# Kernel tuning notes

Measured on AMD Instinct MI355X. Metric: run time of the kernel, lower is better.

The kernel has to match this reference:

```python
import jax, jax.numpy as jnp
import numpy as np

# ---- Cl(4,1) Cayley table (conformal GA: metric +,+,+,+,-) ----
_METRIC = (1.0, 1.0, 1.0, 1.0, -1.0)

def _reorder_sign(a, b):
    # sign from counting swaps to bring blade product to canonical order
    a >>= 1
    s = 0
    while a:
        s += bin(a & b).count("1")
        a >>= 1
    return -1.0 if (s & 1) else 1.0

def _build_cayley():
    C = np.zeros((32, 32, 32), dtype=np.float32)
    for a in range(32):
        for b in range(32):
            s = _reorder_sign(a, b)
            common = a & b
            for i in range(5):
                if (common >> i) & 1:
                    s *= _METRIC[i]
            C[a, b, a ^ b] += s
    return C

CAYLEY = _build_cayley()  # [32,32,32]; out_k = sum_ij C[i,j,k] x_i y_j

EPS = 1e-8

def normalize_cl41(x):
    n = jnp.sqrt(jnp.sum(x * x, axis=-1, keepdims=True))
    return x / (n + EPS)


def setup_inputs() -> dict:
    key = jax.random.key(0)
    k_x, k_wi, k_bi, k_wo, k_bo = jax.random.split(key, 5)
    B, S, D, H = 64, 2048, 6, 8
    x = jax.random.normal(k_x, (B, S, D), dtype=jnp.float32)
    W_in = jax.random.normal(k_wi, (D, H * 32), dtype=jnp.float32) * (1.0 / np.sqrt(D))
    b_in = jax.random.normal(k_bi, (H * 32,), dtype=jnp.float32) * 0.01
    W_out = jax.random.normal(k_wo, (H * 32, 32), dtype=jnp.float32) * (1.0 / np.sqrt(H * 32))
    b_out = jax.random.normal(k_bo, (32,), dtype=jnp.float32) * 0.01
    return {"x": x, "W_in": W_in, "b_in": b_in, "W_out": W_out, "b_out": b_out}


def reference(x, W_in, b_in, W_out, b_out):
    B, S, D = x.shape
    H = W_in.shape[1] // 32
    C = jnp.asarray(CAYLEY)
    # project inputs to per-channel multivectors: (B,S,H,32)
    u = (x @ W_in + b_in).reshape(B, S, H, 32)
    # initial rotor state: identity (scalar blade = 1)
    psi0 = jnp.zeros((B, H, 32), dtype=x.dtype).at[..., 0].set(1.0)

    def step(psi, u_t):  # u_t: (B,H,32)
        delta = normalize_cl41(u_t.at[..., 0].add(1.0))
        psi = normalize_cl41(jnp.einsum("bhi,bhj,ijk->bhk", delta, psi, C))
        return psi, psi

    _, psi_seq = jax.lax.scan(step, psi0, jnp.swapaxes(u, 0, 1))  # (S,B,H,32)
    out = normalize_cl41(psi_seq.reshape(S, B, H * 32) @ W_out + b_out)  # (S,B,32)
    return jnp.swapaxes(out, 0, 1)  # (B,S,32)
```

## Files before the change

kernel.cpp:

```cpp
#include <hip/hip_runtime.h>
#include <hip/hip_bf16.h>
#include <stdint.h>

#define BB 64
#define SS 2048
#define DD 6
#define HH 8
#define NCH 512
#define CHUNKS 256
#define LCH 8

typedef unsigned short ushort_t;
typedef __attribute__((ext_vector_type(8))) __bf16 bf16x8;
typedef __attribute__((ext_vector_type(4))) float f32x4;

struct SignTab { float s[32][32]; };

constexpr int popc5_c(unsigned v) {
    int c = 0;
    for (int i = 0; i < 5; ++i) c += (v >> i) & 1u;
    return c;
}

constexpr SignTab make_signs() {
    SignTab t{};
    for (int a = 0; a < 32; ++a) {
        for (int b = 0; b < 32; ++b) {
            int cnt = 0;
            unsigned aa = ((unsigned)a) >> 1;
            while (aa) { cnt += popc5_c(aa & (unsigned)b); aa >>= 1; }
            if ((a & b) & 16) cnt += 1;
            t.s[a][b] = (cnt & 1) ? -1.0f : 1.0f;
        }
    }
    return t;
}

constexpr SignTab SGN = make_signs();

__device__ __forceinline__ void gp_cl41(const float* __restrict__ a,
                                        const float* __restrict__ b,
                                        float* __restrict__ o) {
#pragma unroll
    for (int k = 0; k < 32; ++k) o[k] = 0.0f;
#pragma unroll
    for (int i = 0; i < 32; ++i) {
#pragma unroll
        for (int k = 0; k < 32; ++k) {
            o[k] = fmaf(SGN.s[i][i ^ k] * a[i], b[i ^ k], o[k]);
        }
    }
}

__device__ __forceinline__ float sumsq32(const float* v) {
    float n0 = 0.f, n1 = 0.f, n2 = 0.f, n3 = 0.f;
#pragma unroll
    for (int k = 0; k < 32; k += 4) {
        n0 = fmaf(v[k+0], v[k+0], n0);
        n1 = fmaf(v[k+1], v[k+1], n1);
        n2 = fmaf(v[k+2], v[k+2], n2);
        n3 = fmaf(v[k+3], v[k+3], n3);
    }
    return (n0 + n1) + (n2 + n3);
}

__device__ __forceinline__ float rsq(float n) {
    return __builtin_amdgcn_rsqf(n);
}

__device__ __forceinline__ uint32_t f2bf_rne(float f) {
    uint32_t u = __float_as_uint(f);
    return (u + 0x7FFFu + ((u >> 16) & 1u)) >> 16;
}

__device__ __forceinline__ void loadp(const float4* __restrict__ a, int stride,
                                      int idx, float* __restrict__ v) {
#pragma unroll
    for (int m = 0; m < 8; ++m) {
        float4 t = a[m * stride + idx];
        v[4*m] = t.x; v[4*m+1] = t.y; v[4*m+2] = t.z; v[4*m+3] = t.w;
    }
}
__device__ __forceinline__ void storep(float4* __restrict__ a, int stride,
                                       int idx, const float* __restrict__ v) {
#pragma unroll
    for (int m = 0; m < 8; ++m)
        a[m * stride + idx] = make_float4(v[4*m], v[4*m+1], v[4*m+2], v[4*m+3]);
}

__device__ __forceinline__ void make_delta2(const float4* __restrict__ sW,
                                            const float* __restrict__ xv,
                                            float* __restrict__ dl0,
                                            float* __restrict__ dl1) {
#pragma unroll
    for (int j4 = 0; j4 < 8; ++j4) {
        float4 bv = sW[48 + j4];
        dl0[4*j4+0] = bv.x; dl0[4*j4+1] = bv.y; dl0[4*j4+2] = bv.z; dl0[4*j4+3] = bv.w;
        dl1[4*j4+0] = bv.x; dl1[4*j4+1] = bv.y; dl1[4*j4+2] = bv.z; dl1[4*j4+3] = bv.w;
    }
#pragma unroll
    for (int d = 0; d < 6; ++d) {
        float a0 = xv[d], a1 = xv[6 + d];
#pragma unroll
        for (int j4 = 0; j4 < 8; ++j4) {
            float4 w = sW[d * 8 + j4];
            dl0[4*j4+0] = fmaf(a0, w.x, dl0[4*j4+0]);
            dl0[4*j4+1] = fmaf(a0, w.y, dl0[4*j4+1]);
            dl0[4*j4+2] = fmaf(a0, w.z, dl0[4*j4+2]);
            dl0[4*j4+3] = fmaf(a0, w.w, dl0[4*j4+3]);
            dl1[4*j4+0] = fmaf(a1, w.x, dl1[4*j4+0]);
            dl1[4*j4+1] = fmaf(a1, w.y, dl1[4*j4+1]);
            dl1[4*j4+2] = fmaf(a1, w.z, dl1[4*j4+2]);
            dl1[4*j4+3] = fmaf(a1, w.w, dl1[4*j4+3]);
        }
    }
    dl0[0] += 1.0f;
    dl1[0] += 1.0f;
}

__device__ __forceinline__ void loadx12(const float* __restrict__ xr, float* __restrict__ xv) {
    const float4* xp = (const float4*)xr;
#pragma unroll
    for (int m = 0; m < 3; ++m) {
        float4 t4 = xp[m];
        xv[4*m] = t4.x; xv[4*m+1] = t4.y; xv[4*m+2] = t4.z; xv[4*m+3] = t4.w;
    }
}

__global__ __launch_bounds__(256, 1) void k_scan(
        const float* __restrict__ x, const float* __restrict__ W_in,
        const float* __restrict__ b_in, float* __restrict__ Ebuf) {
    __shared__ float4 sW4[57];
    __shared__ float4 sTv[8 * CHUNKS];
    __shared__ float4 sUv[8 * 128];
    __shared__ float4 sGv[8 * 64];
    __shared__ float4 sPv[8 * 64];

    int chain = blockIdx.x;
    int b = chain >> 3, h = chain & 7;
    int c = threadIdx.x;

    if (c < 56) {
        float4 v;
        if (c < 48) {
            int d = c / 8, j4 = c % 8;
            const float* p = W_in + d * 256 + h * 32 + 4 * j4;
            v = make_float4(p[0], p[1], p[2], p[3]);
        } else {
            const float* p = b_in + h * 32 + 4 * (c - 48);
            v = make_float4(p[0], p[1], p[2], p[3]);
        }
        sW4[c] = v;
    }
    __syncthreads();

    const float* xrow = x + ((size_t)b * SS + (size_t)c * LCH) * DD;
    float P[32], O[32];
    {
        float xv[12];
        loadx12(xrow, xv);
        float dl0[32], dl1[32];
        make_delta2(sW4, xv, dl0, dl1);
        gp_cl41(dl1, dl0, P);
    }
#pragma unroll 1
    for (int pr = 1; pr < 4; ++pr) {
        float xv[12];
        loadx12(xrow + 12 * pr, xv);
        float dl0[32], dl1[32];
        make_delta2(sW4, xv, dl0, dl1);
        gp_cl41(dl0, P, O);
        gp_cl41(dl1, O, P);
    }
    {
        float inv = rsq(sumsq32(P));
#pragma unroll
        for (int k = 0; k < 32; ++k) P[k] *= inv;
        storep(sTv, CHUNKS, c, P);
    }
    __syncthreads();

    int wave = c >> 6, lane = c & 63;
    int w_act = (blockIdx.x ^ (blockIdx.x >> 8)) & 3;

    if (c < 128) {
        float A_[32], B_[32], U_[32];
        loadp(sTv, CHUNKS, 2 * c + 1, A_);
        loadp(sTv, CHUNKS, 2 * c,     B_);
        gp_cl41(A_, B_, U_);
        storep(sUv, 128, c, U_);
    }
    __syncthreads();

    if (wave == w_act) {
        float A_[32], B_[32], G_[32];
        loadp(sUv, 128, 2 * lane + 1, A_);
        loadp(sUv, 128, 2 * lane,     B_);
        gp_cl41(A_, B_, G_);
        storep(sGv, 64, lane, G_);
    } else if (wave == (w_act ^ 2)) {
        float A_[32], B_[32], P3_[32];
        loadp(sTv, CHUNKS, 4 * lane + 2, A_);
        loadp(sUv, 128, 2 * lane, B_);
        gp_cl41(A_, B_, P3_);
        storep(sPv, 64, lane, P3_);
    }
    __syncthreads();

    {
        bool act = (wave == w_act);
        float gv[32];
        if (act) loadp(sGv, 64, lane, gv);
#pragma unroll 1
        for (int off = 1; off < 64; off <<= 1) {
            if (act && lane >= off) {
                float w_[32], o_[32];
                loadp(sGv, 64, lane - off, w_);
                gp_cl41(gv, w_, o_);
                float inv = rsq(sumsq32(o_));
#pragma unroll
                for (int k = 0; k < 32; ++k) gv[k] = o_[k] * inv;
                storep(sGv, 64, lane, gv);
            }
            __syncthreads();
        }
    }

    {
        int g = c >> 2, r = c & 3;
        float EG[32], E_[32];
        if (g == 0) {
#pragma unroll
            for (int k = 0; k < 32; ++k) EG[k] = (k == 0) ? 1.f : 0.f;
        } else {
            loadp(sGv, 64, g - 1, EG);
        }
        if (r == 0) {
#pragma unroll
            for (int k = 0; k < 32; ++k) E_[k] = EG[k];
        } else {
            float L[32];
            if (r == 1)      loadp(sTv, CHUNKS, c - 1, L);
            else if (r == 2) loadp(sUv, 128, (c - 2) >> 1, L);
            else             loadp(sPv, 64, g, L);
            gp_cl41(L, EG, E_);
        }
        float inv = rsq(sumsq32(E_));
        float4* dst = (float4*)(Ebuf + ((size_t)chain * CHUNKS + c) * 32);
#pragma unroll
        for (int m = 0; m < 8; ++m)
            dst[m] = make_float4(E_[4*m] * inv, E_[4*m+1] * inv,
                                 E_[4*m+2] * inv, E_[4*m+3] * inv);
    }
}

__global__ __launch_bounds__(256, 1) void k_chain_proj(
        const float* __restrict__ x, const float* __restrict__ W_in,
        const float* __restrict__ b_in, const float* __restrict__ Ebuf,
        const float* __restrict__ W_out, const float* __restrict__ b_out,
        float* __restrict__ out) {
    __shared__ float4 sW4[8][57];
    __shared__ float sX[1536];
    __shared__ ushort_t Wt[32 * 256];
    __shared__ ushort_t psiT[4 * 16 * 256];

    int tid = threadIdx.x;
    int wv = tid >> 6, lane = tid & 63;
    int b = blockIdx.x >> 3, gq = blockIdx.x & 7;
    int grp = gq * 4 + wv;
    int c0 = grp * 8;
    int cl = lane >> 3, h = lane & 7;
    int q = lane >> 4, n0 = lane & 15;

    float4 pv[8];
    {
        const float4* ep = (const float4*)(Ebuf +
                (((size_t)b * HH + h) * CHUNKS + (c0 + cl)) * 32);
#pragma unroll
        for (int m = 0; m < 8; ++m) pv[m] = ep[m];
    }

    for (int idx = tid; idx < 448; idx += 256) {
        int hh = idx / 56, r = idx % 56;
        float4 v;
        if (r < 48) {
            int d = r / 8, j4 = r % 8;
            const float* p = W_in + d * 256 + hh * 32 + 4 * j4;
            v = make_float4(p[0], p[1], p[2], p[3]);
        } else {
            const float* p = b_in + hh * 32 + 4 * (r - 48);
            v = make_float4(p[0], p[1], p[2], p[3]);
        }
        sW4[hh][r] = v;
    }

    {
        const float4* xp = (const float4*)(x + ((size_t)b * SS + (size_t)gq * 256) * DD);
        float4* sx4 = (float4*)sX;
        for (int idx = tid; idx < 384; idx += 256) sx4[idx] = xp[idx];
    }

    for (int idx = tid; idx < 2048; idx += 256) {
        int k = idx >> 3, n4 = (idx & 7) << 2;
        float4 w4 = ((const float4*)W_out)[idx];
        ushort_t vals[4] = { (ushort_t)f2bf_rne(w4.x), (ushort_t)f2bf_rne(w4.y),
                             (ushort_t)f2bf_rne(w4.z), (ushort_t)f2bf_rne(w4.w) };
#pragma unroll
        for (int j = 0; j < 4; ++j) {
            int n = n4 + j;
            uint32_t off = (uint32_t)(n * 512 + 2 * k) ^ (uint32_t)((n & 7) << 4);
            *(ushort_t*)((char*)Wt + off) = vals[j];
        }
    }
    __syncthreads();

    float p[32];
#pragma unroll
    for (int m = 0; m < 8; ++m) {
        p[4*m] = pv[m].x; p[4*m+1] = pv[m].y; p[4*m+2] = pv[m].z; p[4*m+3] = pv[m].w;
    }

    bf16x8 Bf[2][8];
#pragma unroll
    for (int nt = 0; nt < 2; ++nt) {
        int n = nt * 16 + n0;
        uint32_t rb = (uint32_t)(n * 512);
        uint32_t sw = (uint32_t)((n & 7) << 4);
#pragma unroll
        for (int kk = 0; kk < 8; ++kk)
            Bf[nt][kk] = *(const bf16x8*)((const char*)Wt + ((rb + kk * 64 + q * 16) ^ sw));
    }
    float bn0 = b_out[n0], bn1 = b_out[16 + n0];

    ushort_t* myT = psiT + wv * 16 * 256;

#pragma unroll 1
    for (int pr = 0; pr < 4; ++pr) {
        float xv[12];
        {
            const float* xr = sX + (wv * 64 + cl * 8 + 2 * pr) * 6;
#pragma unroll
            for (int d = 0; d < 12; ++d) xv[d] = xr[d];
        }

        float dl0[32], dl1[32], o[32];
        make_delta2(sW4[h], xv, dl0, dl1);

        gp_cl41(dl0, p, o);
        {
            float inv = rsq(sumsq32(o));
            int row = cl * 2;
            uint32_t rb = (uint32_t)(row * 512 + h * 64);
            uint32_t sw = (uint32_t)((row & 7) << 4);
            uint32_t pk[16];
#pragma unroll
            for (int m = 0; m < 16; ++m)
                pk[m] = f2bf_rne(o[2*m] * inv) | (f2bf_rne(o[2*m+1] * inv) << 16);
#pragma unroll
            for (int m = 0; m < 4; ++m)
                *(uint4*)((char*)myT + ((rb + 16 * m) ^ sw)) =
                    make_uint4(pk[4*m], pk[4*m+1], pk[4*m+2], pk[4*m+3]);
        }
        gp_cl41(dl1, o, p);
        {
            float inv = rsq(sumsq32(p));
            int row = cl * 2 + 1;
            uint32_t rb = (uint32_t)(row * 512 + h * 64);
            uint32_t sw = (uint32_t)((row & 7) << 4);
            uint32_t pk[16];
#pragma unroll
            for (int m = 0; m < 16; ++m)
                pk[m] = f2bf_rne(p[2*m] * inv) | (f2bf_rne(p[2*m+1] * inv) << 16);
#pragma unroll
            for (int m = 0; m < 4; ++m)
                *(uint4*)((char*)myT + ((rb + 16 * m) ^ sw)) =
                    make_uint4(pk[4*m], pk[4*m+1], pk[4*m+2], pk[4*m+3]);
        }

        __syncthreads();

        f32x4 acc0 = {0.f, 0.f, 0.f, 0.f};
        f32x4 acc1 = {0.f, 0.f, 0.f, 0.f};
        {
            uint32_t rb = (uint32_t)(n0 * 512);
            uint32_t sw = (uint32_t)((n0 & 7) << 4);
#pragma unroll
            for (int kk = 0; kk < 8; ++kk) {
                bf16x8 af = *(const bf16x8*)((const char*)myT + ((rb + kk * 64 + q * 16) ^ sw));
                acc0 = __builtin_amdgcn_mfma_f32_16x16x32_bf16(af, Bf[0][kk], acc0, 0, 0, 0);
                acc1 = __builtin_amdgcn_mfma_f32_16x16x32_bf16(af, Bf[1][kk], acc1, 0, 0, 0);
            }
        }

        float c0v[4], c1v[4], ssq[4];
#pragma unroll
        for (int i = 0; i < 4; ++i) {
            c0v[i] = acc0[i] + bn0;
            c1v[i] = acc1[i] + bn1;
            ssq[i] = c0v[i] * c0v[i] + c1v[i] * c1v[i];
        }
#pragma unroll
        for (int m = 1; m < 16; m <<= 1) {
#pragma unroll
            for (int i = 0; i < 4; ++i) ssq[i] += __shfl_xor(ssq[i], m);
        }
#pragma unroll
        for (int i = 0; i < 4; ++i) {
            float inv = rsq(ssq[i]);
            int mrow = q * 4 + i;
            int s = (c0 + (mrow >> 1)) * LCH + 2 * pr + (mrow & 1);
            size_t row = (size_t)b * SS + s;
            out[row * 32 + n0]      = c0v[i] * inv;
            out[row * 32 + 16 + n0] = c1v[i] * inv;
        }

        __syncthreads();
    }
}

extern "C" void kernel_launch(void* const* d_in, const int* in_sizes, int n_in,
                              void* d_out, int out_size, void* d_ws, size_t ws_size,
                              hipStream_t stream) {
    const float* x     = (const float*)d_in[0];
    const float* W_in  = (const float*)d_in[1];
    const float* b_in  = (const float*)d_in[2];
    const float* W_out = (const float*)d_in[3];
    const float* b_out = (const float*)d_in[4];
    float* out = (float*)d_out;

    float* Ebuf = (float*)d_ws;

    k_scan      <<<NCH, 256, 0, stream>>>(x, W_in, b_in, Ebuf);
    k_chain_proj<<<NCH, 256, 0, stream>>>(x, W_in, b_in, Ebuf, W_out, b_out, out);
}
```

Before: 192.6 us.

## Replace two-level chunk-prefix reduction with full-block Hillis-Steele scan

The chunk-prefix computation in k_scan used to run a pairwise reduction tree, scan 64 group products on a single wave, and then expand them back out per chunk. It now runs a Hillis-Steele inclusive scan over all 256 chunk products using the whole block, and writes exclusive prefixes by shifting outputs by one. Shared storage changes from four transposed float4 arrays to one row-major [256][36] padded array. The scan takes 8 dependent steps instead of about 6 and does far more geometric products, but all four waves stay busy and the tree and expansion phases are gone.

```diff
diff --git a/kernel.cpp b/kernel.cpp
--- a/kernel.cpp
+++ b/kernel.cpp
@@ -71,21 +71,6 @@
 __device__ __forceinline__ uint32_t f2bf_rne(float f) {
     uint32_t u = __float_as_uint(f);
     return (u + 0x7FFFu + ((u >> 16) & 1u)) >> 16;
-}
-
-__device__ __forceinline__ void loadp(const float4* __restrict__ a, int stride,
-                                      int idx, float* __restrict__ v) {
-#pragma unroll
-    for (int m = 0; m < 8; ++m) {
-        float4 t = a[m * stride + idx];
-        v[4*m] = t.x; v[4*m+1] = t.y; v[4*m+2] = t.z; v[4*m+3] = t.w;
-    }
-}
-__device__ __forceinline__ void storep(float4* __restrict__ a, int stride,
-                                       int idx, const float* __restrict__ v) {
-#pragma unroll
-    for (int m = 0; m < 8; ++m)
-        a[m * stride + idx] = make_float4(v[4*m], v[4*m+1], v[4*m+2], v[4*m+3]);
 }
 
 __device__ __forceinline__ void make_delta2(const float4* __restrict__ sW,
@@ -131,10 +116,7 @@
         const float* __restrict__ x, const float* __restrict__ W_in,
         const float* __restrict__ b_in, float* __restrict__ Ebuf) {
     __shared__ float4 sW4[57];
-    __shared__ float4 sTv[8 * CHUNKS];
-    __shared__ float4 sUv[8 * 128];
-    __shared__ float4 sGv[8 * 64];
-    __shared__ float4 sPv[8 * 64];
+    __shared__ float sT[CHUNKS][36];
 
     int chain = blockIdx.x;
     int b = chain >> 3, h = chain & 7;
@@ -172,85 +154,53 @@
         gp_cl41(dl0, P, O);
         gp_cl41(dl1, O, P);
     }
+
+    float v[32];
     {
         float inv = rsq(sumsq32(P));
 #pragma unroll
-        for (int k = 0; k < 32; ++k) P[k] *= inv;
-        storep(sTv, CHUNKS, c, P);
+        for (int k = 0; k < 32; ++k) v[k] = P[k] * inv;
+#pragma unroll
+        for (int m = 0; m < 8; ++m)
+            *(float4*)&sT[c][4*m] = make_float4(v[4*m], v[4*m+1], v[4*m+2], v[4*m+3]);
     }
     __syncthreads();
 
-    int wave = c >> 6, lane = c & 63;
-    int w_act = (blockIdx.x ^ (blockIdx.x >> 8)) & 3;
-
-    if (c < 128) {
-        float A_[32], B_[32], U_[32];
-        loadp(sTv, CHUNKS, 2 * c + 1, A_);
-        loadp(sTv, CHUNKS, 2 * c,     B_);
-        gp_cl41(A_, B_, U_);
-        storep(sUv, 128, c, U_);
-    }
-    __syncthreads();
-
-    if (wave == w_act) {
-        float A_[32], B_[32], G_[32];
-        loadp(sUv, 128, 2 * lane + 1, A_);
-        loadp(sUv, 128, 2 * lane,     B_);
-        gp_cl41(A_, B_, G_);
-        storep(sGv, 64, lane, G_);
-    } else if (wave == (w_act ^ 2)) {
-        float A_[32], B_[32], P3_[32];
-        loadp(sTv, CHUNKS, 4 * lane + 2, A_);
-        loadp(sUv, 128, 2 * lane, B_);
-        gp_cl41(A_, B_, P3_);
-        storep(sPv, 64, lane, P3_);
-    }
-    __syncthreads();
-
-    {
-        bool act = (wave == w_act);
-        float gv[32];
-        if (act) loadp(sGv, 64, lane, gv);
 #pragma unroll 1
-        for (int off = 1; off < 64; off <<= 1) {
-            if (act && lane >= off) {
-                float w_[32], o_[32];
-                loadp(sGv, 64, lane - off, w_);
-                gp_cl41(gv, w_, o_);
-                float inv = rsq(sumsq32(o_));
-#pragma unroll
-                for (int k = 0; k < 32; ++k) gv[k] = o_[k] * inv;
-                storep(sGv, 64, lane, gv);
+    for (int off = 1; off < CHUNKS; off <<= 1) {
+        float w[32];
+        bool act = (c >= off);
+        if (act) {
+#pragma unroll
+            for (int m = 0; m < 8; ++m) {
+                float4 t4 = *(const float4*)&sT[c - off][4*m];
+                w[4*m] = t4.x; w[4*m+1] = t4.y; w[4*m+2] = t4.z; w[4*m+3] = t4.w;
             }
-            __syncthreads();
-        }
-    }
-
-    {
-        int g = c >> 2, r = c & 3;
-        float EG[32], E_[32];
-        if (g == 0) {
-#pragma unroll
-            for (int k = 0; k < 32; ++k) EG[k] = (k == 0) ? 1.f : 0.f;
-        } else {
-            loadp(sGv, 64, g - 1, EG);
-        }
-        if (r == 0) {
-#pragma unroll
-            for (int k = 0; k < 32; ++k) E_[k] = EG[k];
-        } else {
-            float L[32];
-            if (r == 1)      loadp(sTv, CHUNKS, c - 1, L);
-            else if (r == 2) loadp(sUv, 128, (c - 2) >> 1, L);
-            else             loadp(sPv, 64, g, L);
-            gp_cl41(L, EG, E_);
-        }
-        float inv = rsq(sumsq32(E_));
-        float4* dst = (float4*)(Ebuf + ((size_t)chain * CHUNKS + c) * 32);
+        }
+        __syncthreads();
+        if (act) {
+            gp_cl41(v, w, O);
+            float inv = rsq(sumsq32(O));
+#pragma unroll
+            for (int k = 0; k < 32; ++k) v[k] = O[k] * inv;
+#pragma unroll
+            for (int m = 0; m < 8; ++m)
+                *(float4*)&sT[c][4*m] = make_float4(v[4*m], v[4*m+1], v[4*m+2], v[4*m+3]);
+        }
+        __syncthreads();
+    }
+
+    float* dst = Ebuf + (size_t)chain * CHUNKS * 32;
+    if (c == 0) {
+        *(float4*)dst = make_float4(1.f, 0.f, 0.f, 0.f);
+#pragma unroll
+        for (int m = 1; m < 8; ++m) *(float4*)(dst + 4*m) = make_float4(0.f, 0.f, 0.f, 0.f);
+    }
+    if (c < CHUNKS - 1) {
+        float* d2 = dst + (size_t)(c + 1) * 32;
 #pragma unroll
         for (int m = 0; m < 8; ++m)
-            dst[m] = make_float4(E_[4*m] * inv, E_[4*m+1] * inv,
-                                 E_[4*m+2] * inv, E_[4*m+3] * inv);
+            *(float4*)(d2 + 4*m) = make_float4(v[4*m], v[4*m+1], v[4*m+2], v[4*m+3]);
     }
 }
 
```

After: 174.5 us. 9.4% less time.
